# Kernel tuning notes

Measured on AMD Instinct MI355X. Metric: run time of the kernel, lower is better.

## Reference

```python
import jax, jax.numpy as jnp
import numpy as np

D_IN = 2048
D_OUT = 2048
N_HEADS = 32
N_KV = 8
HEAD_DIM = D_OUT // N_HEADS  # 64
CTX = 2048
ROPE_BASE = 10000.0


def _rope_tables(head_dim, ctx, base):
    inv_freq = 1.0 / base ** (np.arange(0, head_dim, 2, dtype=np.float32) / head_dim)
    pos = np.arange(ctx, dtype=np.float32)
    ang = pos[:, None] * inv_freq[None, :]          # [ctx, hd/2]
    ang = np.concatenate([ang, ang], axis=1)         # [ctx, hd]
    return jnp.asarray(np.cos(ang)), jnp.asarray(np.sin(ang))


def _apply_rope(x, cos, sin):
    # x: [b, h, n, hd]; cos/sin: [n, hd]
    half = x.shape[-1] // 2
    x1, x2 = x[..., :half], x[..., half:]
    rotated = jnp.concatenate([-x2, x1], axis=-1)
    return x * cos + rotated * sin


def setup_inputs() -> dict:
    key = jax.random.key(0)
    ks = jax.random.split(key, 5)
    b, n = 1, 2048
    x = jax.random.normal(ks[0], (b, n, D_IN), dtype=jnp.float32)
    s = 0.02
    Wq = jax.random.normal(ks[1], (D_IN, D_OUT), dtype=jnp.float32) * s
    Wk = jax.random.normal(ks[2], (D_IN, N_KV * HEAD_DIM), dtype=jnp.float32) * s
    Wv = jax.random.normal(ks[3], (D_IN, N_KV * HEAD_DIM), dtype=jnp.float32) * s
    Wo = jax.random.normal(ks[4], (D_OUT, D_OUT), dtype=jnp.float32) * s
    cos, sin = _rope_tables(HEAD_DIM, CTX, ROPE_BASE)
    return {"x": x, "Wq": Wq, "Wk": Wk, "Wv": Wv, "Wo": Wo, "cos": cos, "sin": sin}


def reference(x, Wq, Wk, Wv, Wo, cos, sin):
    b, n, _ = x.shape
    gs = N_HEADS // N_KV  # group size
    q = (x @ Wq).reshape(b, n, N_HEADS, HEAD_DIM).transpose(0, 2, 1, 3)  # [b,H,n,d]
    k = (x @ Wk).reshape(b, n, N_KV, HEAD_DIM).transpose(0, 2, 1, 3)     # [b,G,n,d]
    v = (x @ Wv).reshape(b, n, N_KV, HEAD_DIM).transpose(0, 2, 1, 3)
    q = _apply_rope(q, cos[:n], sin[:n])
    k = _apply_rope(k, cos[:n], sin[:n])
    # GQA: view queries as [b, G, gs, n, d]; broadcast K/V over the group axis
    qg = q.reshape(b, N_KV, gs, n, HEAD_DIM)
    scores = jnp.einsum('bgrnd,bgmd->bgrnm', qg, k) / HEAD_DIM ** 0.5
    causal = jnp.triu(jnp.ones((n, n), dtype=bool), k=1)
    scores = jnp.where(causal, -jnp.inf, scores)
    w = jax.nn.softmax(scores, axis=-1)
    ctx = jnp.einsum('bgrnm,bgmd->bgrnd', w, v)           # [b,G,gs,n,d]
    ctx = ctx.reshape(b, N_HEADS, n, HEAD_DIM).transpose(0, 2, 1, 3).reshape(b, n, D_OUT)
    return ctx @ Wo
```

## Files before the change

### kernel.cpp

```cpp
#include <hip/hip_runtime.h>
#include <hip/hip_bf16.h>

typedef __bf16 bf16x8 __attribute__((ext_vector_type(8)));
typedef float f32x4 __attribute__((ext_vector_type(4)));
typedef unsigned u32x4 __attribute__((ext_vector_type(4)));

#define MFMA16 __builtin_amdgcn_mfma_f32_16x16x32_bf16

#define GLD16(gp, lp) __builtin_amdgcn_global_load_lds( \
    (const __attribute__((address_space(1))) void*)(gp), \
    (__attribute__((address_space(3))) void*)(lp), 16, 0, 0)

__device__ __forceinline__ unsigned short f2bf(float f) {
  __hip_bfloat16 h = __float2bfloat16(f);
  return *(unsigned short*)&h;
}
__device__ __forceinline__ float bf2f(unsigned short u) {
  union { unsigned u; float f; } v; v.u = ((unsigned)u) << 16; return v.f;
}

__global__ __launch_bounds__(256)
void convert_bf16_kernel(const float* __restrict__ in, unsigned short* __restrict__ out) {
  int i = blockIdx.x * 256 + threadIdx.x;
  float4 a = *(const float4*)&in[i * 8];
  float4 b = *(const float4*)&in[i * 8 + 4];
  uint4 o;
  o.x = (unsigned)f2bf(a.x) | ((unsigned)f2bf(a.y) << 16);
  o.y = (unsigned)f2bf(a.z) | ((unsigned)f2bf(a.w) << 16);
  o.z = (unsigned)f2bf(b.x) | ((unsigned)f2bf(b.y) << 16);
  o.w = (unsigned)f2bf(b.z) | ((unsigned)f2bf(b.w) << 16);
  *(uint4*)&out[i * 8] = o;
}

__global__ __launch_bounds__(256)
void transpose_bf16_kernel(const float* __restrict__ in, unsigned short* __restrict__ out,
                           int K, int N) {
  __shared__ float tile[64][68];
  const int t = threadIdx.x;
  const int k0 = blockIdx.y * 64, n0 = blockIdx.x * 64;
#pragma unroll
  for (int i = 0; i < 4; ++i) {
    int r = i * 16 + (t >> 4);
    int cc = (t & 15) * 4;
    float4 v = *(const float4*)&in[(k0 + r) * N + n0 + cc];
    tile[r][cc] = v.x; tile[r][cc + 1] = v.y; tile[r][cc + 2] = v.z; tile[r][cc + 3] = v.w;
  }
  __syncthreads();
#pragma unroll
  for (int i = 0; i < 2; ++i) {
    int on = i * 32 + (t >> 3);
    int ok = (t & 7) * 8;
    uint4 o;
    o.x = (unsigned)f2bf(tile[ok + 0][on]) | ((unsigned)f2bf(tile[ok + 1][on]) << 16);
    o.y = (unsigned)f2bf(tile[ok + 2][on]) | ((unsigned)f2bf(tile[ok + 3][on]) << 16);
    o.z = (unsigned)f2bf(tile[ok + 4][on]) | ((unsigned)f2bf(tile[ok + 5][on]) << 16);
    o.w = (unsigned)f2bf(tile[ok + 6][on]) | ((unsigned)f2bf(tile[ok + 7][on]) << 16);
    *(uint4*)&out[(n0 + on) * K + k0 + ok] = o;
  }
}

__global__ __launch_bounds__(256)
void qkv_gemm_kernel(const unsigned short* __restrict__ xb,
                     const unsigned short* __restrict__ Wqt,
                     const unsigned short* __restrict__ Wkt,
                     const unsigned short* __restrict__ Wvt,
                     const float* __restrict__ cosT, const float* __restrict__ sinT,
                     unsigned short* __restrict__ Qb, unsigned short* __restrict__ Kb,
                     unsigned short* __restrict__ Vt)
{
  __shared__ unsigned short Al[2][64 * 64];
  __shared__ unsigned short Bl[2][128 * 64];
  const int t = threadIdx.x;
  const int w = t >> 6, l = t & 63, g = l >> 4, c = l & 15;
  const int wr = w >> 1, wc = w & 1;
  const int r0 = blockIdx.y * 64;
  const int c0 = blockIdx.x * 128;

  const unsigned short* B; int brow0;
  if (c0 < 2048)      { B = Wqt; brow0 = c0; }
  else if (c0 < 2560) { B = Wkt; brow0 = c0 - 2048; }
  else                { B = Wvt; brow0 = c0 - 2560; }

  f32x4 acc[2][4];
#pragma unroll
  for (int m = 0; m < 2; ++m)
#pragma unroll
    for (int n = 0; n < 4; ++n) acc[m][n] = (f32x4){0.f, 0.f, 0.f, 0.f};

  const int srow = t >> 3;
  const int scol = ((t & 7) ^ (srow & 7)) * 8;
  const unsigned dbase = (unsigned)(w * 512);

#define QKV_STAGE(buf, kt_) do {                                              \
    GLD16(&xb[(r0 + srow) * 2048 + (kt_) + scol],        &Al[buf][dbase]);    \
    GLD16(&xb[(r0 + 32 + srow) * 2048 + (kt_) + scol],   &Al[buf][2048 + dbase]); \
    GLD16(&B[(brow0 + srow) * 2048 + (kt_) + scol],      &Bl[buf][dbase]);    \
    GLD16(&B[(brow0 + 32 + srow) * 2048 + (kt_) + scol], &Bl[buf][2048 + dbase]); \
    GLD16(&B[(brow0 + 64 + srow) * 2048 + (kt_) + scol], &Bl[buf][4096 + dbase]); \
    GLD16(&B[(brow0 + 96 + srow) * 2048 + (kt_) + scol], &Bl[buf][6144 + dbase]); \
  } while (0)

  QKV_STAGE(0, 0);
  __syncthreads();

  int cur = 0;
  for (int kt = 0; kt < 2048; kt += 64) {
    if (kt + 64 < 2048) QKV_STAGE(cur ^ 1, kt + 64);
#pragma unroll
    for (int ks = 0; ks < 2; ++ks) {
      const int slot = ((ks * 4 + g) ^ (c & 7)) * 8;
      bf16x8 aF[2], bF[4];
#pragma unroll
      for (int m = 0; m < 2; ++m)
        aF[m] = *(const bf16x8*)&Al[cur][(wr * 32 + m * 16 + c) * 64 + slot];
#pragma unroll
      for (int n = 0; n < 4; ++n)
        bF[n] = *(const bf16x8*)&Bl[cur][(wc * 64 + n * 16 + c) * 64 + slot];
#pragma unroll
      for (int m = 0; m < 2; ++m)
#pragma unroll
        for (int n = 0; n < 4; ++n)
          acc[m][n] = MFMA16(aF[m], bF[n], acc[m][n], 0, 0, 0);
    }
    __syncthreads();
    cur ^= 1;
  }
#undef QKV_STAGE

  const int wcol0 = c0 + wc * 64;
  if (c0 < 2560) {
    unsigned short* dst; int hh;
    if (c0 < 2048) { dst = Qb; hh = wcol0 >> 6; }
    else           { dst = Kb; hh = (wcol0 - 2048) >> 6; }
#pragma unroll
    for (int m = 0; m < 2; ++m) {
#pragma unroll
      for (int j = 0; j < 4; ++j) {
        int p = r0 + wr * 32 + m * 16 + g * 4 + j;
#pragma unroll
        for (int n = 0; n < 2; ++n) {
          int d = n * 16 + c;
          float cv = cosT[p * 64 + d];
          float sv = sinT[p * 64 + d];
          float lo = acc[m][n][j], hi = acc[m][n + 2][j];
          dst[(hh * 2048 + p) * 64 + d]      = f2bf(lo * cv - hi * sv);
          dst[(hh * 2048 + p) * 64 + d + 32] = f2bf(hi * cv + lo * sv);
        }
      }
    }
  } else {
    int kvh = (wcol0 - 2560) >> 6;
#pragma unroll
    for (int m = 0; m < 2; ++m) {
      int p0 = r0 + wr * 32 + m * 16 + g * 4;
      int ps = (p0 & ~0x1C) | ((p0 & 0x0C) << 1) | ((p0 & 0x10) >> 2);
#pragma unroll
      for (int n = 0; n < 4; ++n) {
        int d = n * 16 + c;
        ushort4 u;
        u.x = f2bf(acc[m][n][0]); u.y = f2bf(acc[m][n][1]);
        u.z = f2bf(acc[m][n][2]); u.w = f2bf(acc[m][n][3]);
        *(ushort4*)&Vt[(kvh * 64 + d) * 2048 + ps] = u;
      }
    }
  }
}

__global__ __launch_bounds__(256)
void attn_kernel(const unsigned short* __restrict__ Qb,
                 const unsigned short* __restrict__ Kb,
                 const unsigned short* __restrict__ Vt,
                 unsigned short* __restrict__ pA, unsigned short* __restrict__ pB,
                 float* __restrict__ lsA, float* __restrict__ lsB)
{
  __shared__ unsigned short Kl[2][64 * 64];
  __shared__ unsigned short Vl[2][64 * 64];
  const int t = threadIdx.x, w = t >> 6, l = t & 63, g = l >> 4, c = l & 15;

  static const int qt_order[16] = {15,14,13,12, 0,1,2,3, 11,10,9,8, 4,5,6,7};
  const int b = blockIdx.x;
  const int h = b & 31;
  const int half = (b >> 5) & 1;
  const int qt = qt_order[b >> 6];
  const int kvh = h >> 2;
  const int qb = qt * 128 + w * 32;
  const int t0 = half * (qt + 1);
  const int t1 = t0 + (qt + 1);
  const int myNT = (qb + 32 + 63) >> 6;

  const float C1 = 0.18033688f;
  const float MB = 23.0831067f;

  const int sr1 = t >> 3;
  const int sr2 = sr1 + 32;
  const int sc1 = ((t & 7) ^ (sr1 & 7)) * 8;
  const int sc2 = ((t & 7) ^ (sr2 & 7)) * 8;
  const unsigned ld1 = (unsigned)t * 8;
  const unsigned ld2 = ld1 + 2048;

  const unsigned short* Kh = Kb + kvh * 2048 * 64;
  const unsigned short* Vh = Vt + kvh * 64 * 2048;

#define ATTN_STAGE(buf, nb_) do {                                  \
    GLD16(&Kh[((nb_) + sr1) * 64 + sc1], &Kl[buf][ld1]);           \
    GLD16(&Kh[((nb_) + sr2) * 64 + sc2], &Kl[buf][ld2]);           \
    GLD16(&Vh[sr1 * 2048 + (nb_) + sc1], &Vl[buf][ld1]);           \
    GLD16(&Vh[sr2 * 2048 + (nb_) + sc2], &Vl[buf][ld2]);           \
  } while (0)

  bf16x8 qf[2][2];
#pragma unroll
  for (int m = 0; m < 2; ++m)
#pragma unroll
    for (int ks = 0; ks < 2; ++ks)
      qf[m][ks] = *(const bf16x8*)&Qb[(h * 2048 + qb + m * 16 + c) * 64 + ks * 32 + g * 8];

  f32x4 ctx[2][4];
  float lsum[2] = {0.f, 0.f};
#pragma unroll
  for (int m = 0; m < 2; ++m)
#pragma unroll
    for (int n = 0; n < 4; ++n) ctx[m][n] = (f32x4){0.f, 0.f, 0.f, 0.f};

  ATTN_STAGE(0, t0 * 64);
  __syncthreads();

  int cur = 0;
  for (int ti = t0; ti < t1; ++ti) {
    if (ti + 1 < t1) ATTN_STAGE(cur ^ 1, (ti + 1) * 64);

    if (ti < myNT) {
      const int kvb = ti * 64;

      f32x4 ST[4][2];
#pragma unroll
      for (int nn = 0; nn < 4; ++nn)
#pragma unroll
        for (int m = 0; m < 2; ++m) ST[nn][m] = (f32x4){0.f, 0.f, 0.f, 0.f};

      __builtin_amdgcn_s_setprio(1);
#pragma unroll
      for (int ks = 0; ks < 2; ++ks) {
        bf16x8 kF[4];
#pragma unroll
        for (int nn = 0; nn < 4; ++nn) {
          int slot = (ks * 4 + g) ^ (c & 7);
          kF[nn] = *(const bf16x8*)&Kl[cur][(nn * 16 + c) * 64 + slot * 8];
        }
#pragma unroll
        for (int nn = 0; nn < 4; ++nn)
#pragma unroll
          for (int m = 0; m < 2; ++m)
            ST[nn][m] = MFMA16(kF[nn], qf[m][ks], ST[nn][m], 0, 0, 0);
      }
      __builtin_amdgcn_s_setprio(0);

      if (kvb + 63 > qb) {
#pragma unroll
        for (int nn = 0; nn < 4; ++nn)
#pragma unroll
          for (int j = 0; j < 4; ++j) {
            int kpos = kvb + nn * 16 + g * 4 + j;
#pragma unroll
            for (int m = 0; m < 2; ++m) {
              int qpos = qb + m * 16 + c;
              if (kpos > qpos) ST[nn][m][j] = -1e30f;
            }
          }
      }

#pragma unroll
      for (int nn = 0; nn < 4; ++nn)
#pragma unroll
        for (int m = 0; m < 2; ++m)
#pragma unroll
          for (int j = 0; j < 4; ++j) {
            float p = exp2f(fmaf(ST[nn][m][j], C1, -MB));
            ST[nn][m][j] = p;
            lsum[m] += p;
          }

      unsigned pk[4][2][2];
#pragma unroll
      for (int nn = 0; nn < 4; ++nn)
#pragma unroll
        for (int m = 0; m < 2; ++m) {
          pk[nn][m][0] = (unsigned)f2bf(ST[nn][m][0]) | ((unsigned)f2bf(ST[nn][m][1]) << 16);
          pk[nn][m][1] = (unsigned)f2bf(ST[nn][m][2]) | ((unsigned)f2bf(ST[nn][m][3]) << 16);
        }

      bf16x8 pa[2][2];
#pragma unroll
      for (int m = 0; m < 2; ++m)
#pragma unroll
        for (int ks = 0; ks < 2; ++ks) {
          u32x4 pw;
          pw[0] = pk[2 * ks][m][0];
          pw[1] = pk[2 * ks][m][1];
          pw[2] = pk[2 * ks + 1][m][0];
          pw[3] = pk[2 * ks + 1][m][1];
          union { u32x4 u; bf16x8 b; } cvt; cvt.u = pw;
          pa[m][ks] = cvt.b;
        }

      __builtin_amdgcn_s_setprio(1);
#pragma unroll
      for (int ks = 0; ks < 2; ++ks) {
        bf16x8 vF[4];
#pragma unroll
        for (int n = 0; n < 4; ++n) {
          int slot = (ks * 4 + g) ^ (c & 7);
          vF[n] = *(const bf16x8*)&Vl[cur][(n * 16 + c) * 64 + slot * 8];
        }
#pragma unroll
        for (int m = 0; m < 2; ++m)
#pragma unroll
          for (int n = 0; n < 4; ++n)
            ctx[m][n] = MFMA16(pa[m][ks], vF[n], ctx[m][n], 0, 0, 0);
      }
      __builtin_amdgcn_s_setprio(0);
    }

    __syncthreads();
    cur ^= 1;
  }
#undef ATTN_STAGE

  unsigned short* pOut = half ? pB : pA;
  float* lsOut = half ? lsB : lsA;

#pragma unroll
  for (int m = 0; m < 2; ++m) {
    float rs = lsum[m];
    rs += __shfl_xor(rs, 16);
    rs += __shfl_xor(rs, 32);
    if (l < 16) lsOut[h * 2048 + qb + m * 16 + l] = rs;
  }
#pragma unroll
  for (int m = 0; m < 2; ++m)
#pragma unroll
    for (int n = 0; n < 4; ++n)
#pragma unroll
      for (int j = 0; j < 4; ++j) {
        int p = qb + m * 16 + g * 4 + j;
        int d = n * 16 + c;
        pOut[p * 2048 + h * 64 + d] = f2bf(ctx[m][n][j]);
      }
}

__global__ __launch_bounds__(256)
void combine_kernel(const unsigned short* __restrict__ pA,
                    unsigned short* __restrict__ pB_out,
                    const float* __restrict__ lsA, const float* __restrict__ lsB)
{
  const int idx = (blockIdx.x * 256 + threadIdx.x) * 8;
  const int p = idx >> 11;
  const int col = idx & 2047;
  const int h = col >> 6;
  const float inv = 1.f / (lsA[h * 2048 + p] + lsB[h * 2048 + p]);

  ushort4 a0 = *(const ushort4*)&pA[idx];
  ushort4 a1 = *(const ushort4*)&pA[idx + 4];
  ushort4 b0 = *(const ushort4*)&pB_out[idx];
  ushort4 b1 = *(const ushort4*)&pB_out[idx + 4];
  ushort4 o0, o1;
  o0.x = f2bf((bf2f(a0.x) + bf2f(b0.x)) * inv);
  o0.y = f2bf((bf2f(a0.y) + bf2f(b0.y)) * inv);
  o0.z = f2bf((bf2f(a0.z) + bf2f(b0.z)) * inv);
  o0.w = f2bf((bf2f(a0.w) + bf2f(b0.w)) * inv);
  o1.x = f2bf((bf2f(a1.x) + bf2f(b1.x)) * inv);
  o1.y = f2bf((bf2f(a1.y) + bf2f(b1.y)) * inv);
  o1.z = f2bf((bf2f(a1.z) + bf2f(b1.z)) * inv);
  o1.w = f2bf((bf2f(a1.w) + bf2f(b1.w)) * inv);
  *(ushort4*)&pB_out[idx]     = o0;
  *(ushort4*)&pB_out[idx + 4] = o1;
}

__global__ __launch_bounds__(256)
void out_gemm_kernel(const unsigned short* __restrict__ ctxB,
                     const unsigned short* __restrict__ Wot,
                     float* __restrict__ out)
{
  __shared__ unsigned short Al[2][64 * 64];
  __shared__ unsigned short Bl[2][128 * 64];
  const int t = threadIdx.x;
  const int w = t >> 6, l = t & 63, g = l >> 4, c = l & 15;
  const int wr = w >> 1, wc = w & 1;
  const int r0 = blockIdx.y * 64;
  const int c0 = blockIdx.x * 128;

  f32x4 acc[2][4];
#pragma unroll
  for (int m = 0; m < 2; ++m)
#pragma unroll
    for (int n = 0; n < 4; ++n) acc[m][n] = (f32x4){0.f, 0.f, 0.f, 0.f};

  const int srow = t >> 3;
  const int scol = ((t & 7) ^ (srow & 7)) * 8;
  const unsigned dbase = (unsigned)(w * 512);

#define OUT_STAGE(buf, kt_) do {                                               \
    GLD16(&ctxB[(r0 + srow) * 2048 + (kt_) + scol],      &Al[buf][dbase]);     \
    GLD16(&ctxB[(r0 + 32 + srow) * 2048 + (kt_) + scol], &Al[buf][2048 + dbase]); \
    GLD16(&Wot[(c0 + srow) * 2048 + (kt_) + scol],       &Bl[buf][dbase]);     \
    GLD16(&Wot[(c0 + 32 + srow) * 2048 + (kt_) + scol],  &Bl[buf][2048 + dbase]); \
    GLD16(&Wot[(c0 + 64 + srow) * 2048 + (kt_) + scol],  &Bl[buf][4096 + dbase]); \
    GLD16(&Wot[(c0 + 96 + srow) * 2048 + (kt_) + scol],  &Bl[buf][6144 + dbase]); \
  } while (0)

  OUT_STAGE(0, 0);
  __syncthreads();

  int cur = 0;
  for (int kt = 0; kt < 2048; kt += 64) {
    if (kt + 64 < 2048) OUT_STAGE(cur ^ 1, kt + 64);
#pragma unroll
    for (int ks = 0; ks < 2; ++ks) {
      const int slot = ((ks * 4 + g) ^ (c & 7)) * 8;
      bf16x8 aF[2], bF[4];
#pragma unroll
      for (int m = 0; m < 2; ++m)
        aF[m] = *(const bf16x8*)&Al[cur][(wr * 32 + m * 16 + c) * 64 + slot];
#pragma unroll
      for (int n = 0; n < 4; ++n)
        bF[n] = *(const bf16x8*)&Bl[cur][(wc * 64 + n * 16 + c) * 64 + slot];
#pragma unroll
      for (int m = 0; m < 2; ++m)
#pragma unroll
        for (int n = 0; n < 4; ++n)
          acc[m][n] = MFMA16(aF[m], bF[n], acc[m][n], 0, 0, 0);
    }
    __syncthreads();
    cur ^= 1;
  }
#undef OUT_STAGE

#pragma unroll
  for (int m = 0; m < 2; ++m)
#pragma unroll
    for (int j = 0; j < 4; ++j) {
      int p = r0 + wr * 32 + m * 16 + g * 4 + j;
#pragma unroll
      for (int n = 0; n < 4; ++n)
        out[p * 2048 + c0 + wc * 64 + n * 16 + c] = acc[m][n][j];
    }
}

extern "C" void kernel_launch(void* const* d_in, const int* in_sizes, int n_in,
                              void* d_out, int out_size, void* d_ws, size_t ws_size,
                              hipStream_t stream) {
  const float* x    = (const float*)d_in[0];
  const float* Wq   = (const float*)d_in[1];
  const float* Wk   = (const float*)d_in[2];
  const float* Wv   = (const float*)d_in[3];
  const float* Wo   = (const float*)d_in[4];
  const float* cosT = (const float*)d_in[5];
  const float* sinT = (const float*)d_in[6];
  float* out = (float*)d_out;

  unsigned short* xb   = (unsigned short*)d_ws;
  unsigned short* pA   = xb;
  unsigned short* Wot  = xb;
  unsigned short* Wqt  = xb + 4 * 1024 * 1024;
  unsigned short* ctxB = Wqt;
  unsigned short* Wkt  = Wqt + 4 * 1024 * 1024;
  float*          lsA  = (float*)Wkt;
  unsigned short* Wvt  = Wkt + 1024 * 1024;
  float*          lsB  = (float*)Wvt;
  unsigned short* Qb   = Wvt + 1024 * 1024;
  unsigned short* Kb   = Qb + 4 * 1024 * 1024;
  unsigned short* Vt   = Kb + 1024 * 1024;

  convert_bf16_kernel<<<2048, 256, 0, stream>>>(x, xb);
  transpose_bf16_kernel<<<dim3(32, 32), 256, 0, stream>>>(Wq, Wqt, 2048, 2048);
  transpose_bf16_kernel<<<dim3(8, 32), 256, 0, stream>>>(Wk, Wkt, 2048, 512);
  transpose_bf16_kernel<<<dim3(8, 32), 256, 0, stream>>>(Wv, Wvt, 2048, 512);

  qkv_gemm_kernel<<<dim3(24, 32), 256, 0, stream>>>(xb, Wqt, Wkt, Wvt, cosT, sinT, Qb, Kb, Vt);

  attn_kernel<<<1024, 256, 0, stream>>>(Qb, Kb, Vt, pA, ctxB, lsA, lsB);
  combine_kernel<<<2048, 256, 0, stream>>>(pA, ctxB, lsA, lsB);

  transpose_bf16_kernel<<<dim3(32, 32), 256, 0, stream>>>(Wo, Wot, 2048, 2048);
  out_gemm_kernel<<<dim3(16, 32), 256, 0, stream>>>(ctxB, Wot, out);
}
```

Measured before the change: 136.2 us.

## Split attention KV ranges into 1-3 chunks by query tile for balanced work

Replaces the uniform two-way KV split per query tile with a variable split: early query tiles get one chunk, middle tiles two, late tiles three, for 32 chunk slots per head, ordered by a static schedule. The first chunk writes directly into the context buffer, extra chunks go to a compact side buffer, and the combine kernel sums a variable number of partials. This is meant to even out per-block work under the causal mask and cut partial-buffer traffic for short tiles. In exchange it adds a more complex, branchy combine step and depends on the hand-tuned schedule.

```diff
diff --git a/kernel.cpp b/kernel.cpp
--- a/kernel.cpp
+++ b/kernel.cpp
@@ -170,22 +170,30 @@
 void attn_kernel(const unsigned short* __restrict__ Qb,
                  const unsigned short* __restrict__ Kb,
                  const unsigned short* __restrict__ Vt,
-                 unsigned short* __restrict__ pA, unsigned short* __restrict__ pB,
-                 float* __restrict__ lsA, float* __restrict__ lsB)
+                 unsigned short* __restrict__ ctxB,
+                 unsigned short* __restrict__ pExtra,
+                 float* __restrict__ ls)
 {
   __shared__ unsigned short Kl[2][64 * 64];
   __shared__ unsigned short Vl[2][64 * 64];
   const int t = threadIdx.x, w = t >> 6, l = t & 63, g = l >> 4, c = l & 15;
 
-  static const int qt_order[16] = {15,14,13,12, 0,1,2,3, 11,10,9,8, 4,5,6,7};
+  static const int slot2cid[32] = {15,16,30,31, 4,13,14,25,26,27,28,29,
+                                   11,12,21,22,23,24, 3,9,10,17,18,19,20,
+                                   7,8, 2,5,6, 1, 0};
   const int b = blockIdx.x;
   const int h = b & 31;
-  const int half = (b >> 5) & 1;
-  const int qt = qt_order[b >> 6];
+  const int cid = slot2cid[b >> 5];
+  int qt, ci, k;
+  if (cid < 5)       { qt = cid;                ci = 0;              k = 1; }
+  else if (cid < 17) { qt = 5 + (cid - 5) / 2;  ci = (cid - 5) & 1;  k = 2; }
+  else               { qt = 11 + (cid - 17) / 3; ci = (cid - 17) % 3; k = 3; }
+  const int NT = 2 * qt + 2;
+  const int t0 = (ci * NT) / k;
+  const int t1 = ((ci + 1) * NT) / k;
+
   const int kvh = h >> 2;
   const int qb = qt * 128 + w * 32;
-  const int t0 = half * (qt + 1);
-  const int t1 = t0 + (qt + 1);
   const int myNT = (qb + 32 + 63) >> 6;
 
   const float C1 = 0.18033688f;
@@ -326,15 +334,23 @@
   }
 #undef ATTN_STAGE
 
-  unsigned short* pOut = half ? pB : pA;
-  float* lsOut = half ? lsB : lsA;
+  unsigned short* pOut; int prstride;
+  if (ci == 0) {
+    pOut = ctxB + (qt * 128) * 2048 + h * 64;
+    prstride = 2048;
+  } else {
+    int eo = (qt < 11) ? (qt - 5) : (2 * qt - 16);
+    pOut = pExtra + (h * 16 + eo + ci - 1) * 8192;
+    prstride = 64;
+  }
+  float* lsOut = ls + (h * 32 + cid) * 128;
 
 #pragma unroll
   for (int m = 0; m < 2; ++m) {
     float rs = lsum[m];
     rs += __shfl_xor(rs, 16);
     rs += __shfl_xor(rs, 32);
-    if (l < 16) lsOut[h * 2048 + qb + m * 16 + l] = rs;
+    if (l < 16) lsOut[w * 32 + m * 16 + l] = rs;
   }
 #pragma unroll
   for (int m = 0; m < 2; ++m)
@@ -342,38 +358,53 @@
     for (int n = 0; n < 4; ++n)
 #pragma unroll
       for (int j = 0; j < 4; ++j) {
-        int p = qb + m * 16 + g * 4 + j;
+        int lr = w * 32 + m * 16 + g * 4 + j;
         int d = n * 16 + c;
-        pOut[p * 2048 + h * 64 + d] = f2bf(ctx[m][n][j]);
+        pOut[lr * prstride + d] = f2bf(ctx[m][n][j]);
       }
 }
 
 __global__ __launch_bounds__(256)
-void combine_kernel(const unsigned short* __restrict__ pA,
-                    unsigned short* __restrict__ pB_out,
-                    const float* __restrict__ lsA, const float* __restrict__ lsB)
+void combine_kernel(unsigned short* __restrict__ ctxB,
+                    const unsigned short* __restrict__ pExtra,
+                    const float* __restrict__ ls)
 {
   const int idx = (blockIdx.x * 256 + threadIdx.x) * 8;
   const int p = idx >> 11;
   const int col = idx & 2047;
   const int h = col >> 6;
-  const float inv = 1.f / (lsA[h * 2048 + p] + lsB[h * 2048 + p]);
-
-  ushort4 a0 = *(const ushort4*)&pA[idx];
-  ushort4 a1 = *(const ushort4*)&pA[idx + 4];
-  ushort4 b0 = *(const ushort4*)&pB_out[idx];
-  ushort4 b1 = *(const ushort4*)&pB_out[idx + 4];
+  const int d = col & 63;
+  const int qt = p >> 7;
+  const int lr = p & 127;
+
+  const int k    = (qt < 5) ? 1 : (qt < 11) ? 2 : 3;
+  const int cid0 = (qt < 5) ? qt : (qt < 11) ? (2 * qt - 5) : (3 * qt - 16);
+  const int eo   = (qt < 11) ? (qt - 5) : (2 * qt - 16);
+
+  float a[8];
+  ushort4 c0 = *(const ushort4*)&ctxB[idx];
+  ushort4 c1 = *(const ushort4*)&ctxB[idx + 4];
+  a[0] = bf2f(c0.x); a[1] = bf2f(c0.y); a[2] = bf2f(c0.z); a[3] = bf2f(c0.w);
+  a[4] = bf2f(c1.x); a[5] = bf2f(c1.y); a[6] = bf2f(c1.z); a[7] = bf2f(c1.w);
+  float lt = ls[(h * 32 + cid0) * 128 + lr];
+
+  for (int ci = 1; ci < k; ++ci) {
+    lt += ls[(h * 32 + cid0 + ci) * 128 + lr];
+    const unsigned short* e = &pExtra[(h * 16 + eo + ci - 1) * 8192 + lr * 64 + d];
+    ushort4 e0 = *(const ushort4*)&e[0];
+    ushort4 e1 = *(const ushort4*)&e[4];
+    a[0] += bf2f(e0.x); a[1] += bf2f(e0.y); a[2] += bf2f(e0.z); a[3] += bf2f(e0.w);
+    a[4] += bf2f(e1.x); a[5] += bf2f(e1.y); a[6] += bf2f(e1.z); a[7] += bf2f(e1.w);
+  }
+
+  const float inv = 1.f / lt;
   ushort4 o0, o1;
-  o0.x = f2bf((bf2f(a0.x) + bf2f(b0.x)) * inv);
-  o0.y = f2bf((bf2f(a0.y) + bf2f(b0.y)) * inv);
-  o0.z = f2bf((bf2f(a0.z) + bf2f(b0.z)) * inv);
-  o0.w = f2bf((bf2f(a0.w) + bf2f(b0.w)) * inv);
-  o1.x = f2bf((bf2f(a1.x) + bf2f(b1.x)) * inv);
-  o1.y = f2bf((bf2f(a1.y) + bf2f(b1.y)) * inv);
-  o1.z = f2bf((bf2f(a1.z) + bf2f(b1.z)) * inv);
-  o1.w = f2bf((bf2f(a1.w) + bf2f(b1.w)) * inv);
-  *(ushort4*)&pB_out[idx]     = o0;
-  *(ushort4*)&pB_out[idx + 4] = o1;
+  o0.x = f2bf(a[0] * inv); o0.y = f2bf(a[1] * inv);
+  o0.z = f2bf(a[2] * inv); o0.w = f2bf(a[3] * inv);
+  o1.x = f2bf(a[4] * inv); o1.y = f2bf(a[5] * inv);
+  o1.z = f2bf(a[6] * inv); o1.w = f2bf(a[7] * inv);
+  *(ushort4*)&ctxB[idx]     = o0;
+  *(ushort4*)&ctxB[idx + 4] = o1;
 }
 
 __global__ __launch_bounds__(256)
@@ -458,18 +489,17 @@
   const float* sinT = (const float*)d_in[6];
   float* out = (float*)d_out;
 
-  unsigned short* xb   = (unsigned short*)d_ws;
-  unsigned short* pA   = xb;
-  unsigned short* Wot  = xb;
-  unsigned short* Wqt  = xb + 4 * 1024 * 1024;
-  unsigned short* ctxB = Wqt;
-  unsigned short* Wkt  = Wqt + 4 * 1024 * 1024;
-  float*          lsA  = (float*)Wkt;
-  unsigned short* Wvt  = Wkt + 1024 * 1024;
-  float*          lsB  = (float*)Wvt;
-  unsigned short* Qb   = Wvt + 1024 * 1024;
-  unsigned short* Kb   = Qb + 4 * 1024 * 1024;
-  unsigned short* Vt   = Kb + 1024 * 1024;
+  unsigned short* xb     = (unsigned short*)d_ws;
+  unsigned short* pExtra = xb;
+  unsigned short* Wot    = xb;
+  unsigned short* Wqt    = xb + 4 * 1024 * 1024;
+  unsigned short* ctxB   = Wqt;
+  unsigned short* Wkt    = Wqt + 4 * 1024 * 1024;
+  float*          ls     = (float*)Wkt;
+  unsigned short* Wvt    = Wkt + 1024 * 1024;
+  unsigned short* Qb     = Wvt + 1024 * 1024;
+  unsigned short* Kb     = Qb + 4 * 1024 * 1024;
+  unsigned short* Vt     = Kb + 1024 * 1024;
 
   convert_bf16_kernel<<<2048, 256, 0, stream>>>(x, xb);
   transpose_bf16_kernel<<<dim3(32, 32), 256, 0, stream>>>(Wq, Wqt, 2048, 2048);
@@ -478,8 +508,8 @@
 
   qkv_gemm_kernel<<<dim3(24, 32), 256, 0, stream>>>(xb, Wqt, Wkt, Wvt, cosT, sinT, Qb, Kb, Vt);
 
-  attn_kernel<<<1024, 256, 0, stream>>>(Qb, Kb, Vt, pA, ctxB, lsA, lsB);
-  combine_kernel<<<2048, 256, 0, stream>>>(pA, ctxB, lsA, lsB);
+  attn_kernel<<<1024, 256, 0, stream>>>(Qb, Kb, Vt, ctxB, pExtra, ls);
+  combine_kernel<<<2048, 256, 0, stream>>>(ctxB, pExtra, ls);
 
   transpose_bf16_kernel<<<dim3(32, 32), 256, 0, stream>>>(Wo, Wot, 2048, 2048);
   out_gemm_kernel<<<dim3(16, 32), 256, 0, stream>>>(ctxB, Wot, out);
```

Measured after the change: 140.5 us. +3.2%, slower.
